# Optimization experiments

Measured on AMD Instinct MI355X. Metric: run time of the kernel, lower is better.

## Reference

```python
import jax, jax.numpy as jnp
import numpy as np

B, M, S = 4, 1024, 1024
D, H, FF = 1024, 16, 4096
NE, P = 128, 1
HD = D // H
EPS = 1e-5


def _layer_norm(x, g, b):
    mu = x.mean(-1, keepdims=True)
    var = ((x - mu) ** 2).mean(-1, keepdims=True)
    return (x - mu) * jax.lax.rsqrt(var + EPS) * g + b


def _mha(q_in, kv_in, in_w, in_b, out_w, out_b):
    # torch nn.MultiheadAttention: packed in_proj_weight [3D, D], y = x @ W.T + b
    wq, wk, wv = in_w[:D], in_w[D:2 * D], in_w[2 * D:]
    bq, bk, bv = in_b[:D], in_b[D:2 * D], in_b[2 * D:]
    q = (q_in @ wq.T + bq).reshape(q_in.shape[0], q_in.shape[1], H, HD)
    k = (kv_in @ wk.T + bk).reshape(kv_in.shape[0], kv_in.shape[1], H, HD)
    v = (kv_in @ wv.T + bv).reshape(kv_in.shape[0], kv_in.shape[1], H, HD)
    scores = jnp.einsum('bqhd,bkhd->bhqk', q, k) / jnp.sqrt(jnp.float32(HD))
    attn = jax.nn.softmax(scores, axis=-1)
    o = jnp.einsum('bhqk,bkhd->bqhd', attn, v).reshape(q_in.shape[0], q_in.shape[1], D)
    return o @ out_w.T + out_b


def _soft_moe(h, phi, exp_w, exp_b):
    # h: [b, m, FF]; phi: [FF, n, p]
    logits = jnp.einsum('bmd,dnp->bmnp', h, phi)
    dispatch = jax.nn.softmax(logits, axis=1)  # over tokens m
    b, m, n, p = logits.shape
    combine = jax.nn.softmax(logits.reshape(b, m, n * p), axis=-1).reshape(b, m, n, p)
    slots = jnp.einsum('bmd,bmnp->bnpd', h, dispatch)  # [b, n, p, FF]
    y = jnp.einsum('bnpd,ndo->bnpo', slots, exp_w) + exp_b[None, :, None, :]  # [b, n, p, D]
    return jnp.einsum('bnpo,bmnp->bmo', y, combine)


def setup_inputs() -> dict:
    key = jax.random.key(0)
    ks = jax.random.split(key, 16)
    sc = 0.02

    def rn(k, shape):
        return jax.random.normal(k, shape, jnp.float32) * sc

    return {
        'tgt': jax.random.normal(ks[0], (B, M, D), jnp.float32),
        'memory': jax.random.normal(ks[1], (B, S, D), jnp.float32),
        'sa_in_w': rn(ks[2], (3 * D, D)), 'sa_in_b': jnp.zeros((3 * D,), jnp.float32),
        'sa_out_w': rn(ks[3], (D, D)), 'sa_out_b': jnp.zeros((D,), jnp.float32),
        'ca_in_w': rn(ks[4], (3 * D, D)), 'ca_in_b': jnp.zeros((3 * D,), jnp.float32),
        'ca_out_w': rn(ks[5], (D, D)), 'ca_out_b': jnp.zeros((D,), jnp.float32),
        'norm1_g': jnp.ones((D,), jnp.float32), 'norm1_b': jnp.zeros((D,), jnp.float32),
        'norm2_g': jnp.ones((D,), jnp.float32), 'norm2_b': jnp.zeros((D,), jnp.float32),
        'norm3_g': jnp.ones((D,), jnp.float32), 'norm3_b': jnp.zeros((D,), jnp.float32),
        'lin_w': rn(ks[6], (FF, D)), 'lin_b': jnp.zeros((FF,), jnp.float32),
        'phi': rn(ks[7], (FF, NE, P)),
        'exp_w': rn(ks[8], (NE, FF, D)), 'exp_b': jnp.zeros((NE, D), jnp.float32),
    }


def reference(tgt, memory, sa_in_w, sa_in_b, sa_out_w, sa_out_b,
              ca_in_w, ca_in_b, ca_out_w, ca_out_b,
              norm1_g, norm1_b, norm2_g, norm2_b, norm3_g, norm3_b,
              lin_w, lin_b, phi, exp_w, exp_b):
    # post-norm (norm_first=False), dropout=0 (eval)
    x = tgt
    x = _layer_norm(x + _mha(x, x, sa_in_w, sa_in_b, sa_out_w, sa_out_b), norm1_g, norm1_b)
    x = _layer_norm(x + _mha(x, memory, ca_in_w, ca_in_b, ca_out_w, ca_out_b), norm2_g, norm2_b)
    h = jax.nn.relu(x @ lin_w.T + lin_b)  # [B, M, FF]
    ff = _soft_moe(h, phi, exp_w, exp_b)  # [B, M, D]
    x = _layer_norm(x + ff, norm3_g, norm3_b)
    return x
```

## Files before the change

### kernel.cpp

```cpp
#include <hip/hip_runtime.h>
#include <cstdint>
#include <cstddef>

typedef unsigned short u16;
typedef unsigned int   u32;
typedef short bf16x8 __attribute__((ext_vector_type(8)));
typedef float f32x4  __attribute__((ext_vector_type(4)));
typedef u16   u16x8  __attribute__((ext_vector_type(8)));
typedef u16   u16x4  __attribute__((ext_vector_type(4)));
typedef u16   u16x2  __attribute__((ext_vector_type(2)));

constexpr int B_  = 4;
constexpr int M_  = 1024;
constexpr int S_  = 1024;
constexpr int D_  = 1024;
constexpr int H_  = 16;
constexpr int FF_ = 4096;
constexpr int NE_ = 128;

__device__ __forceinline__ u16 f2bf(float f) {
    u32 u = __builtin_bit_cast(u32, f);
    u = (u + 0x7fffu + ((u >> 16) & 1u)) >> 16;
    return (u16)u;
}
__device__ __forceinline__ float bf2f(u16 u) {
    u32 x = ((u32)u) << 16;
    return __builtin_bit_cast(float, x);
}
__device__ __forceinline__ void gload_lds16(const u16* g, u16* l) {
    __builtin_amdgcn_global_load_lds(
        (const __attribute__((address_space(1))) u32*)g,
        (__attribute__((address_space(3))) u32*)l, 16, 0, 0);
}

template<int OUT_BF16, int RELU, int HAS_BIAS>
__global__ __launch_bounds__(256) void gemm_bt_mfma(
    const u16* __restrict__ A, const u16* __restrict__ W,
    const float* __restrict__ bias, void* __restrict__ Cout,
    int K, int N, int lda, int ldw,
    size_t sA, size_t sW, size_t sC)
{
    __shared__ u16 As[128 * 32];
    __shared__ u16 Bs[128 * 32];
    const int tid = threadIdx.x;
    const int w = tid >> 6, l = tid & 63;
    const int bm = blockIdx.y * 128, bn = blockIdx.x * 128;
    const u16* Ab = A + (size_t)blockIdx.z * sA;
    const u16* Wb = W + (size_t)blockIdx.z * sW;

    const int wr = w >> 1, wc = w & 1;
    const int sr = l >> 2;
    const int sk = (l & 3) * 8;
    const u16* aG0 = Ab + (size_t)(bm + w * 16 + sr) * lda + sk;
    const u16* aG1 = Ab + (size_t)(bm + (w + 4) * 16 + sr) * lda + sk;
    const u16* bG0 = Wb + (size_t)(bn + w * 16 + sr) * ldw + sk;
    const u16* bG1 = Wb + (size_t)(bn + (w + 4) * 16 + sr) * ldw + sk;
    u16* aL0 = &As[w * 512];
    u16* aL1 = &As[(w + 4) * 512];
    u16* bL0 = &Bs[w * 512];
    u16* bL1 = &Bs[(w + 4) * 512];

    const int fr = l & 15;
    const int fk = (l >> 4) * 8;

    f32x4 acc[4][4];
#pragma unroll
    for (int i = 0; i < 4; ++i)
#pragma unroll
        for (int j = 0; j < 4; ++j)
#pragma unroll
            for (int q = 0; q < 4; ++q) acc[i][j][q] = 0.f;

    for (int k0 = 0; k0 < K; k0 += 32) {
        __syncthreads();
        gload_lds16(aG0, aL0);
        gload_lds16(aG1, aL1);
        gload_lds16(bG0, bL0);
        gload_lds16(bG1, bL1);
        aG0 += 32; aG1 += 32; bG0 += 32; bG1 += 32;
        __syncthreads();
        bf16x8 af[4], bfr[4];
#pragma unroll
        for (int m = 0; m < 4; ++m)
            af[m] = *(const bf16x8*)&As[(wr * 64 + m * 16 + fr) * 32 + fk];
#pragma unroll
        for (int n = 0; n < 4; ++n)
            bfr[n] = *(const bf16x8*)&Bs[(wc * 64 + n * 16 + fr) * 32 + fk];
#pragma unroll
        for (int m = 0; m < 4; ++m)
#pragma unroll
            for (int n = 0; n < 4; ++n)
                acc[m][n] = __builtin_amdgcn_mfma_f32_16x16x32_bf16(
                    af[m], bfr[n], acc[m][n], 0, 0, 0);
    }

    const int row0 = bm + wr * 64 + (l >> 4) * 4;
    const int col0 = bn + wc * 64;
#pragma unroll
    for (int n = 0; n < 4; ++n) {
        const int col = col0 + n * 16 + fr;
        float bv = 0.f;
        if (HAS_BIAS) bv = bias[col];
#pragma unroll
        for (int m = 0; m < 4; ++m) {
            const int row = row0 + m * 16;
#pragma unroll
            for (int j = 0; j < 4; ++j) {
                float v = acc[m][n][j] + bv;
                if (RELU) v = fmaxf(v, 0.f);
                const size_t idx = (size_t)blockIdx.z * sC + (size_t)(row + j) * N + col;
                if (OUT_BF16) ((u16*)Cout)[idx] = f2bf(v);
                else          ((float*)Cout)[idx] = v;
            }
        }
    }
}

__global__ __launch_bounds__(256) void flash_attn_kernel(
    const u16* __restrict__ Q, int qs,
    const u16* __restrict__ K, int ks,
    const u16* __restrict__ V, int vs,
    u16* __restrict__ O, int Slen)
{
    __shared__ u16 Qs[64][72];
    __shared__ u16 Ks[64][72];
    __shared__ u16 Vt[64][72];
    __shared__ u16 Pw[4][16][72];
    const int b = blockIdx.z, hh = blockIdx.y;
    const int m0 = blockIdx.x * 64;
    const int tid = threadIdx.x;
    const int w = tid >> 6, l = tid & 63;
    const int lq = l & 15, g = l >> 4;

    {
        const int row = tid >> 2, cg = (tid & 3) * 16;
        const u16* qp = Q + ((size_t)b * M_ + m0 + row) * qs + hh * 64 + cg;
        u16x8 v0 = *(const u16x8*)qp;
        u16x8 v1 = *(const u16x8*)(qp + 8);
        u16x8 o0, o1;
#pragma unroll
        for (int i = 0; i < 8; ++i) {
            o0[i] = f2bf(bf2f(v0[i]) * 0.125f);
            o1[i] = f2bf(bf2f(v1[i]) * 0.125f);
        }
        *(u16x8*)&Qs[row][cg]     = o0;
        *(u16x8*)&Qs[row][cg + 8] = o1;
    }
    __syncthreads();
    bf16x8 qf[2];
    qf[0] = *(const bf16x8*)&Qs[w * 16 + lq][g * 8];
    qf[1] = *(const bf16x8*)&Qs[w * 16 + lq][32 + g * 8];

    f32x4 acc_o[4];
#pragma unroll
    for (int nb = 0; nb < 4; ++nb)
#pragma unroll
        for (int j = 0; j < 4; ++j) acc_o[nb][j] = 0.f;
    float m_run = -1e30f, l_run = 0.f;

    const int kp = tid & 31, dg = tid >> 5;
    const int krow = tid >> 2, kcg = (tid & 3) * 16;

    for (int s0 = 0; s0 < Slen; s0 += 64) {
        __syncthreads();
        {
            const u16* kpp = K + ((size_t)b * Slen + s0 + krow) * ks + hh * 64 + kcg;
            *(u16x8*)&Ks[krow][kcg]     = *(const u16x8*)kpp;
            *(u16x8*)&Ks[krow][kcg + 8] = *(const u16x8*)(kpp + 8);
        }
        {
            const u16* vp0 = V + ((size_t)b * Slen + s0 + 2 * kp) * vs + hh * 64 + dg * 8;
            const u16* vp1 = vp0 + vs;
            u16x8 a = *(const u16x8*)vp0;
            u16x8 c = *(const u16x8*)vp1;
#pragma unroll
            for (int i = 0; i < 8; ++i) {
                u16x2 pk; pk[0] = a[i]; pk[1] = c[i];
                *(u16x2*)&Vt[dg * 8 + i][2 * kp] = pk;
            }
        }
        __syncthreads();

        f32x4 s4[4];
#pragma unroll
        for (int mb = 0; mb < 4; ++mb) {
            f32x4 z = {0.f, 0.f, 0.f, 0.f};
            bf16x8 a0 = *(const bf16x8*)&Ks[mb * 16 + lq][g * 8];
            bf16x8 a1 = *(const bf16x8*)&Ks[mb * 16 + lq][32 + g * 8];
            z = __builtin_amdgcn_mfma_f32_16x16x32_bf16(a0, qf[0], z, 0, 0, 0);
            z = __builtin_amdgcn_mfma_f32_16x16x32_bf16(a1, qf[1], z, 0, 0, 0);
            s4[mb] = z;
        }

        float pm = -1e30f;
#pragma unroll
        for (int mb = 0; mb < 4; ++mb)
#pragma unroll
            for (int j = 0; j < 4; ++j) pm = fmaxf(pm, s4[mb][j]);
        pm = fmaxf(pm, __shfl_xor(pm, 16));
        pm = fmaxf(pm, __shfl_xor(pm, 32));

        u16 pbf[4][4];
        float ls = 0.f;
        if (__all(pm - m_run <= 8.f)) {
#pragma unroll
            for (int mb = 0; mb < 4; ++mb)
#pragma unroll
                for (int j = 0; j < 4; ++j) {
                    float p = __expf(s4[mb][j] - m_run);
                    ls += p;
                    pbf[mb][j] = f2bf(p);
                }
            ls += __shfl_xor(ls, 16);
            ls += __shfl_xor(ls, 32);
            l_run += ls;
        } else {
            const float m_new = fmaxf(m_run, pm);
            const float alpha = __expf(m_run - m_new);
#pragma unroll
            for (int mb = 0; mb < 4; ++mb)
#pragma unroll
                for (int j = 0; j < 4; ++j) {
                    float p = __expf(s4[mb][j] - m_new);
                    ls += p;
                    pbf[mb][j] = f2bf(p);
                }
            ls += __shfl_xor(ls, 16);
            ls += __shfl_xor(ls, 32);
            l_run = l_run * alpha + ls;
            m_run = m_new;
            float al[4];
#pragma unroll
            for (int j = 0; j < 4; ++j) al[j] = __shfl(alpha, 4 * g + j);
#pragma unroll
            for (int nb = 0; nb < 4; ++nb)
#pragma unroll
                for (int j = 0; j < 4; ++j) acc_o[nb][j] *= al[j];
        }

#pragma unroll
        for (int mb = 0; mb < 4; ++mb) {
            u16x4 pk;
            pk[0] = pbf[mb][0]; pk[1] = pbf[mb][1];
            pk[2] = pbf[mb][2]; pk[3] = pbf[mb][3];
            *(u16x4*)&Pw[w][lq][mb * 16 + g * 4] = pk;
        }

#pragma unroll
        for (int kc = 0; kc < 2; ++kc) {
            bf16x8 pa = *(const bf16x8*)&Pw[w][lq][kc * 32 + g * 8];
#pragma unroll
            for (int nb = 0; nb < 4; ++nb) {
                bf16x8 bv = *(const bf16x8*)&Vt[nb * 16 + lq][kc * 32 + g * 8];
                acc_o[nb] = __builtin_amdgcn_mfma_f32_16x16x32_bf16(pa, bv, acc_o[nb], 0, 0, 0);
            }
        }
    }

    float linv[4];
#pragma unroll
    for (int j = 0; j < 4; ++j) linv[j] = 1.f / __shfl(l_run, 4 * g + j);
#pragma unroll
    for (int nb = 0; nb < 4; ++nb)
#pragma unroll
        for (int j = 0; j < 4; ++j) {
            const size_t row = (size_t)b * M_ + m0 + w * 16 + 4 * g + j;
            O[row * D_ + hh * 64 + nb * 16 + lq] = f2bf(acc_o[nb][j] * linv[j]);
        }
}

__global__ __launch_bounds__(256) void cvt_multi_kernel(
    const float* __restrict__ s0, u16* __restrict__ d0,
    const float* __restrict__ s1, u16* __restrict__ d1,
    const float* __restrict__ s2, u16* __restrict__ d2,
    const float* __restrict__ s3, u16* __restrict__ d3,
    const float* __restrict__ s4, u16* __restrict__ d4,
    const float* __restrict__ s5, u16* __restrict__ d5,
    const float* __restrict__ s6, u16* __restrict__ d6)
{
    int blk = blockIdx.x;
    const float* s; u16* d;
    if      (blk < 2048) { s = s0; d = d0; }
    else if (blk < 4096) { s = s1; d = d1; blk -= 2048; }
    else if (blk < 5632) { s = s2; d = d2; blk -= 4096; }
    else if (blk < 6144) { s = s3; d = d3; blk -= 5632; }
    else if (blk < 7680) { s = s4; d = d4; blk -= 6144; }
    else if (blk < 8192) { s = s5; d = d5; blk -= 7680; }
    else                 { s = s6; d = d6; blk -= 8192; }
    const size_t i = ((size_t)blk * 256 + threadIdx.x) * 8;
    float4 a = *(const float4*)(s + i);
    float4 b = *(const float4*)(s + i + 4);
    u16x8 o;
    o[0] = f2bf(a.x); o[1] = f2bf(a.y); o[2] = f2bf(a.z); o[3] = f2bf(a.w);
    o[4] = f2bf(b.x); o[5] = f2bf(b.y); o[6] = f2bf(b.z); o[7] = f2bf(b.w);
    *(u16x8*)(d + i) = o;
}

__global__ __launch_bounds__(256) void transpose_f32_bf16_kernel(
    const float* __restrict__ src, u16* __restrict__ dst, int R, int C,
    size_t sI, size_t sO)
{
    __shared__ u16 t[32][33];
    src += (size_t)blockIdx.z * sI;
    dst += (size_t)blockIdx.z * sO;
    const int c0 = blockIdx.x * 32, r0 = blockIdx.y * 32;
    const int x = threadIdx.x & 31, y = threadIdx.x >> 5;
    for (int i = y; i < 32; i += 8)
        t[i][x] = f2bf(src[(size_t)(r0 + i) * C + c0 + x]);
    __syncthreads();
    for (int i = y; i < 32; i += 8)
        dst[(size_t)(c0 + i) * R + r0 + x] = t[x][i];
}

__global__ __launch_bounds__(256) void transpose_bf16_kernel(
    const u16* __restrict__ src, u16* __restrict__ dst, int R, int C,
    size_t sI, size_t sO)
{
    __shared__ u16 t[32][33];
    src += (size_t)blockIdx.z * sI;
    dst += (size_t)blockIdx.z * sO;
    const int c0 = blockIdx.x * 32, r0 = blockIdx.y * 32;
    const int x = threadIdx.x & 31, y = threadIdx.x >> 5;
    for (int i = y; i < 32; i += 8)
        t[i][x] = src[(size_t)(r0 + i) * C + c0 + x];
    __syncthreads();
    for (int i = y; i < 32; i += 8)
        dst[(size_t)(c0 + i) * R + r0 + x] = t[x][i];
}

__global__ __launch_bounds__(256) void resid_ln_kernel(
    const float* __restrict__ X, const float* __restrict__ R,
    const float* __restrict__ g, const float* __restrict__ bt,
    float* __restrict__ Y, u16* __restrict__ Ybf)
{
    __shared__ float s1[4], s2[4];
    const size_t row = blockIdx.x;
    const int tid = threadIdx.x;
    const float4 x4 = *(const float4*)(X + row * 1024 + tid * 4);
    const float4 r4 = *(const float4*)(R + row * 1024 + tid * 4);
    float v[4] = {x4.x + r4.x, x4.y + r4.y, x4.z + r4.z, x4.w + r4.w};
    float s = v[0] + v[1] + v[2] + v[3];
    float q = v[0] * v[0] + v[1] * v[1] + v[2] * v[2] + v[3] * v[3];
#pragma unroll
    for (int off = 32; off; off >>= 1) {
        s += __shfl_xor(s, off);
        q += __shfl_xor(q, off);
    }
    if ((tid & 63) == 0) { s1[tid >> 6] = s; s2[tid >> 6] = q; }
    __syncthreads();
    s = s1[0] + s1[1] + s1[2] + s1[3];
    q = s2[0] + s2[1] + s2[2] + s2[3];
    const float mu = s * (1.f / 1024.f);
    const float var = q * (1.f / 1024.f) - mu * mu;
    const float rinv = rsqrtf(var + 1e-5f);
    const float4 g4 = *(const float4*)(g + tid * 4);
    const float4 b4 = *(const float4*)(bt + tid * 4);
    float o[4];
    o[0] = (v[0] - mu) * rinv * g4.x + b4.x;
    o[1] = (v[1] - mu) * rinv * g4.y + b4.y;
    o[2] = (v[2] - mu) * rinv * g4.z + b4.z;
    o[3] = (v[3] - mu) * rinv * g4.w + b4.w;
    *(float4*)(Y + row * 1024 + tid * 4) = *(float4*)o;
    if (Ybf) {
        u16x4 ob;
        ob[0] = f2bf(o[0]); ob[1] = f2bf(o[1]);
        ob[2] = f2bf(o[2]); ob[3] = f2bf(o[3]);
        *(u16x4*)(Ybf + row * 1024 + tid * 4) = ob;
    }
}

__global__ __launch_bounds__(256) void dispatch_softmax_T_kernel(
    const float* __restrict__ logitsP, u16* __restrict__ dispT)
{
    __shared__ float red[4];
    constexpr size_t CH = (size_t)B_ * M_ * NE_;
    const int n = blockIdx.x, b = blockIdx.y;
    u16* O = dispT + ((size_t)b * NE_ + n) * M_;
    const int tid = threadIdx.x;
    float v[4];
#pragma unroll
    for (int i = 0; i < 4; ++i) {
        const size_t idx = (size_t)(b * M_ + tid + 256 * i) * NE_ + n;
        v[i] = logitsP[idx] + logitsP[CH + idx] + logitsP[2 * CH + idx] + logitsP[3 * CH + idx];
    }
    float mx = fmaxf(fmaxf(v[0], v[1]), fmaxf(v[2], v[3]));
#pragma unroll
    for (int off = 32; off; off >>= 1) mx = fmaxf(mx, __shfl_xor(mx, off));
    if ((tid & 63) == 0) red[tid >> 6] = mx;
    __syncthreads();
    mx = fmaxf(fmaxf(red[0], red[1]), fmaxf(red[2], red[3]));
    __syncthreads();
    float e[4], s = 0.f;
#pragma unroll
    for (int i = 0; i < 4; ++i) { e[i] = __expf(v[i] - mx); s += e[i]; }
#pragma unroll
    for (int off = 32; off; off >>= 1) s += __shfl_xor(s, off);
    if ((tid & 63) == 0) red[tid >> 6] = s;
    __syncthreads();
    s = red[0] + red[1] + red[2] + red[3];
    const float inv = 1.f / s;
#pragma unroll
    for (int i = 0; i < 4; ++i) O[tid + 256 * i] = f2bf(e[i] * inv);
}

__global__ __launch_bounds__(64) void combine_softmax_kernel(
    const float* __restrict__ logitsP, u16* __restrict__ comb)
{
    constexpr size_t CH = (size_t)B_ * M_ * NE_;
    const size_t row = blockIdx.x;
    const int lane = threadIdx.x;
    const size_t i0 = row * NE_ + lane;
    const size_t i1 = i0 + 64;
    float a = logitsP[i0] + logitsP[CH + i0] + logitsP[2 * CH + i0] + logitsP[3 * CH + i0];
    float c = logitsP[i1] + logitsP[CH + i1] + logitsP[2 * CH + i1] + logitsP[3 * CH + i1];
    float mx = fmaxf(a, c);
#pragma unroll
    for (int off = 32; off; off >>= 1) mx = fmaxf(mx, __shfl_xor(mx, off));
    float e0 = __expf(a - mx), e1 = __expf(c - mx);
    float s = e0 + e1;
#pragma unroll
    for (int off = 32; off; off >>= 1) s += __shfl_xor(s, off);
    const float inv = 1.f / s;
    comb[row * NE_ + lane]      = f2bf(e0 * inv);
    comb[row * NE_ + lane + 64] = f2bf(e1 * inv);
}

__global__ __launch_bounds__(256) void expert_partial_kernel(
    const float* __restrict__ slots, const float* __restrict__ exp_w,
    float* __restrict__ part)
{
    __shared__ float sl[4][512];
    const int n = blockIdx.x;
    const int c = blockIdx.y;
    const int f0 = c * 512;
    const int t = threadIdx.x;
    for (int i = t; i < 2048; i += 256) {
        const int b = i >> 9, f = i & 511;
        sl[b][f] = slots[((size_t)b * NE_ + n) * FF_ + f0 + f];
    }
    __syncthreads();
    const int d4 = t * 4;
    const float* wp = exp_w + ((size_t)n * FF_ + f0) * D_ + d4;
    f32x4 acc[4];
#pragma unroll
    for (int b = 0; b < 4; ++b)
#pragma unroll
        for (int j = 0; j < 4; ++j) acc[b][j] = 0.f;
#pragma unroll 4
    for (int f = 0; f < 512; ++f) {
        const float4 w4 = *(const float4*)wp;
        wp += D_;
#pragma unroll
        for (int b = 0; b < 4; ++b) {
            const float s = sl[b][f];
            acc[b][0] = fmaf(s, w4.x, acc[b][0]);
            acc[b][1] = fmaf(s, w4.y, acc[b][1]);
            acc[b][2] = fmaf(s, w4.z, acc[b][2]);
            acc[b][3] = fmaf(s, w4.w, acc[b][3]);
        }
    }
#pragma unroll
    for (int b = 0; b < 4; ++b)
        *(f32x4*)&part[(((size_t)c * 4 + b) * NE_ + n) * D_ + d4] = acc[b];
}

__global__ __launch_bounds__(256) void reduce_yT_kernel(
    const float* __restrict__ part, const float* __restrict__ exp_b,
    u16* __restrict__ yT)
{
    __shared__ float tile[32][33];
    const int d0 = blockIdx.x * 32, n0 = blockIdx.y * 32, b = blockIdx.z;
    const int x = threadIdx.x & 31, y = threadIdx.x >> 5;
    for (int i = y; i < 32; i += 8) {
        const int n = n0 + i;
        float s = exp_b[(size_t)n * D_ + d0 + x];
#pragma unroll
        for (int c = 0; c < 8; ++c)
            s += part[(((size_t)c * 4 + b) * NE_ + n) * D_ + d0 + x];
        tile[i][x] = s;
    }
    __syncthreads();
    for (int i = y; i < 32; i += 8)
        yT[((size_t)b * D_ + d0 + i) * NE_ + n0 + x] = f2bf(tile[x][i]);
}

extern "C" void kernel_launch(void* const* d_in, const int* in_sizes, int n_in,
                              void* d_out, int out_size, void* d_ws, size_t ws_size,
                              hipStream_t stream)
{
    const float* tgt      = (const float*)d_in[0];
    const float* memry    = (const float*)d_in[1];
    const float* sa_in_w  = (const float*)d_in[2];
    const float* sa_in_b  = (const float*)d_in[3];
    const float* sa_out_w = (const float*)d_in[4];
    const float* sa_out_b = (const float*)d_in[5];
    const float* ca_in_w  = (const float*)d_in[6];
    const float* ca_in_b  = (const float*)d_in[7];
    const float* ca_out_w = (const float*)d_in[8];
    const float* ca_out_b = (const float*)d_in[9];
    const float* norm1_g  = (const float*)d_in[10];
    const float* norm1_b  = (const float*)d_in[11];
    const float* norm2_g  = (const float*)d_in[12];
    const float* norm2_b  = (const float*)d_in[13];
    const float* norm3_g  = (const float*)d_in[14];
    const float* norm3_b  = (const float*)d_in[15];
    const float* lin_w    = (const float*)d_in[16];
    const float* lin_b    = (const float*)d_in[17];
    const float* phi      = (const float*)d_in[18];
    const float* exp_w    = (const float*)d_in[19];
    const float* exp_b    = (const float*)d_in[20];

    float* ws = (float*)d_ws;
    u16*   qkv_bf  = (u16*)(ws);
    float* proj    = ws + 6291456;
    float* x1      = ws + 10485760;
    float* x2      = ws + 14680064;
    float* logitsP = ws + 18874368;
    float* part    = ws + 20971520;
    u16*   h_bf    = (u16*)(ws + 25165824);
    u16*   hT_bf   = (u16*)(ws + 33554432);
    u16*   obuf_bf = (u16*)(ws + 41943040);
    u16*   x1_bf   = (u16*)(ws + 44040192);
    u16*   x2_bf   = (u16*)(ws + 46137344);
    u16*   tgt_bf  = (u16*)(ws + 48234496);
    u16*   mem_bf  = (u16*)(ws + 50331648);
    u16*   dispT   = (u16*)(ws + 52428800);
    u16*   comb_bf = (u16*)(ws + 52690944);
    u16*   yT_bf   = (u16*)(ws + 52953088);
    u16*   slots_n = 0; float* slots = ws + 53215232;
    (void)slots_n;
    u16*   w_sa_in = (u16*)(ws + 55312384);
    u16*   w_sa_out= (u16*)(ws + 56885248);
    u16*   w_ca_in = (u16*)(ws + 57409536);
    u16*   w_ca_out= (u16*)(ws + 58982400);
    u16*   w_lin   = (u16*)(ws + 59506688);
    u16*   phiT    = (u16*)(ws + 61603840);

    cvt_multi_kernel<<<10240, 256, 0, stream>>>(
        tgt, tgt_bf, memry, mem_bf, sa_in_w, w_sa_in, sa_out_w, w_sa_out,
        ca_in_w, w_ca_in, ca_out_w, w_ca_out, lin_w, w_lin);
    transpose_f32_bf16_kernel<<<dim3(4, 128, 1), 256, 0, stream>>>(phi, phiT, 4096, 128, 0, 0);

    gemm_bt_mfma<1, 0, 1><<<dim3(24, 32, 1), 256, 0, stream>>>(
        tgt_bf, w_sa_in, sa_in_b, qkv_bf, 1024, 3072, 1024, 1024, 0, 0, 0);
    flash_attn_kernel<<<dim3(16, 16, 4), 256, 0, stream>>>(
        qkv_bf, 3072, qkv_bf + 1024, 3072, qkv_bf + 2048, 3072, obuf_bf, S_);
    gemm_bt_mfma<0, 0, 1><<<dim3(8, 32, 1), 256, 0, stream>>>(
        obuf_bf, w_sa_out, sa_out_b, proj, 1024, 1024, 1024, 1024, 0, 0, 0);
    resid_ln_kernel<<<4096, 256, 0, stream>>>(tgt, proj, norm1_g, norm1_b, x1, x1_bf);

    u16* qca_bf = qkv_bf;
    u16* kvca_bf = qkv_bf + (size_t)4096 * 1024;
    gemm_bt_mfma<1, 0, 1><<<dim3(8, 32, 1), 256, 0, stream>>>(
        x1_bf, w_ca_in, ca_in_b, qca_bf, 1024, 1024, 1024, 1024, 0, 0, 0);
    gemm_bt_mfma<1, 0, 1><<<dim3(16, 32, 1), 256, 0, stream>>>(
        mem_bf, w_ca_in + (size_t)1024 * 1024, ca_in_b + 1024,
        kvca_bf, 1024, 2048, 1024, 1024, 0, 0, 0);
    flash_attn_kernel<<<dim3(16, 16, 4), 256, 0, stream>>>(
        qca_bf, 1024, kvca_bf, 2048, kvca_bf + 1024, 2048, obuf_bf, S_);
    gemm_bt_mfma<0, 0, 1><<<dim3(8, 32, 1), 256, 0, stream>>>(
        obuf_bf, w_ca_out, ca_out_b, proj, 1024, 1024, 1024, 1024, 0, 0, 0);
    resid_ln_kernel<<<4096, 256, 0, stream>>>(x1, proj, norm2_g, norm2_b, x2, x2_bf);

    gemm_bt_mfma<1, 1, 1><<<dim3(32, 32, 1), 256, 0, stream>>>(
        x2_bf, w_lin, lin_b, h_bf, 1024, 4096, 1024, 1024, 0, 0, 0);
    gemm_bt_mfma<0, 0, 0><<<dim3(1, 32, 4), 256, 0, stream>>>(
        h_bf, phiT, nullptr, logitsP, 1024, 128, 4096, 4096,
        1024, 1024, (size_t)B_ * M_ * NE_);
    dispatch_softmax_T_kernel<<<dim3(NE_, B_), 256, 0, stream>>>(logitsP, dispT);
    combine_softmax_kernel<<<dim3(B_ * M_), 64, 0, stream>>>(logitsP, comb_bf);
    transpose_bf16_kernel<<<dim3(128, 32, 4), 256, 0, stream>>>(
        h_bf, hT_bf, 1024, 4096, (size_t)M_ * FF_, (size_t)M_ * FF_);
    gemm_bt_mfma<0, 0, 0><<<dim3(32, 1, 4), 256, 0, stream>>>(
        dispT, hT_bf, nullptr, slots, 1024, 4096, 1024, 1024,
        (size_t)NE_ * M_, (size_t)FF_ * M_, (size_t)NE_ * FF_);
    expert_partial_kernel<<<dim3(NE_, 8), 256, 0, stream>>>(slots, exp_w, part);
    reduce_yT_kernel<<<dim3(32, 4, 4), 256, 0, stream>>>(part, exp_b, yT_bf);
    gemm_bt_mfma<0, 0, 0><<<dim3(8, 8, 4), 256, 0, stream>>>(
        comb_bf, yT_bf, nullptr, proj, 128, 1024, 128, 128,
        (size_t)M_ * NE_, (size_t)D_ * NE_, (size_t)M_ * D_);
    resid_ln_kernel<<<4096, 256, 0, stream>>>(x2, proj, norm3_g, norm3_b,
                                              (float*)d_out, nullptr);
}
```

Baseline: 839.0 us.

## Use 64x128 GEMM tiles with swizzled LDS, fuse h transpose, double-buffer attention

The GEMM kernel now uses 64-row by 128-column tiles with an XOR-swizzled LDS layout to reduce bank conflicts, and the grids are doubled to give more blocks per launch. The linear+ReLU GEMM also writes a transposed bf16 copy of h directly, which removes the separate transpose kernel and its extra pass over memory. Flash attention keeps Q in registers instead of staging it through LDS and double-buffers the K/V tiles, prefetching the next tile into registers while the current one is computed. In exchange, the smaller tiles lower per-block data reuse, and the transposed store in the GEMM epilogue is strided.

```diff
diff --git a/kernel.cpp b/kernel.cpp
--- a/kernel.cpp
+++ b/kernel.cpp
@@ -33,84 +33,86 @@
         (__attribute__((address_space(3))) u32*)l, 16, 0, 0);
 }
 
-template<int OUT_BF16, int RELU, int HAS_BIAS>
-__global__ __launch_bounds__(256) void gemm_bt_mfma(
+template<int OUT_BF16, int RELU, int HAS_BIAS, int WRITE_HT>
+__global__ __launch_bounds__(256) void gemm64_mfma(
     const u16* __restrict__ A, const u16* __restrict__ W,
     const float* __restrict__ bias, void* __restrict__ Cout,
+    u16* __restrict__ HT,
     int K, int N, int lda, int ldw,
     size_t sA, size_t sW, size_t sC)
 {
-    __shared__ u16 As[128 * 32];
+    __shared__ u16 As[64 * 32];
     __shared__ u16 Bs[128 * 32];
     const int tid = threadIdx.x;
     const int w = tid >> 6, l = tid & 63;
-    const int bm = blockIdx.y * 128, bn = blockIdx.x * 128;
+    const int fr = l & 15, g = l >> 4;
+    const int bm = blockIdx.y * 64, bn = blockIdx.x * 128;
     const u16* Ab = A + (size_t)blockIdx.z * sA;
     const u16* Wb = W + (size_t)blockIdx.z * sW;
 
-    const int wr = w >> 1, wc = w & 1;
-    const int sr = l >> 2;
-    const int sk = (l & 3) * 8;
-    const u16* aG0 = Ab + (size_t)(bm + w * 16 + sr) * lda + sk;
-    const u16* aG1 = Ab + (size_t)(bm + (w + 4) * 16 + sr) * lda + sk;
-    const u16* bG0 = Wb + (size_t)(bn + w * 16 + sr) * ldw + sk;
-    const u16* bG1 = Wb + (size_t)(bn + (w + 4) * 16 + sr) * ldw + sk;
-    u16* aL0 = &As[w * 512];
-    u16* aL1 = &As[(w + 4) * 512];
+    const int qcol = ((l & 3) ^ ((l >> 3) & 3)) * 8;
+    const int srow = w * 16 + (l >> 2);
+    const u16* aG  = Ab + (size_t)(bm + srow) * lda + qcol;
+    const u16* bG0 = Wb + (size_t)(bn + srow) * ldw + qcol;
+    const u16* bG1 = bG0 + (size_t)64 * ldw;
+    u16* aL  = &As[w * 512];
     u16* bL0 = &Bs[w * 512];
-    u16* bL1 = &Bs[(w + 4) * 512];
-
-    const int fr = l & 15;
-    const int fk = (l >> 4) * 8;
-
-    f32x4 acc[4][4];
-#pragma unroll
-    for (int i = 0; i < 4; ++i)
-#pragma unroll
-        for (int j = 0; j < 4; ++j)
-#pragma unroll
-            for (int q = 0; q < 4; ++q) acc[i][j][q] = 0.f;
+    u16* bL1 = &Bs[2048 + w * 512];
+
+    const int qsw = (g ^ ((fr >> 1) & 3)) * 8;
+
+    f32x4 acc[4][2];
+#pragma unroll
+    for (int m = 0; m < 4; ++m)
+#pragma unroll
+        for (int n = 0; n < 2; ++n)
+#pragma unroll
+            for (int q = 0; q < 4; ++q) acc[m][n][q] = 0.f;
 
     for (int k0 = 0; k0 < K; k0 += 32) {
         __syncthreads();
-        gload_lds16(aG0, aL0);
-        gload_lds16(aG1, aL1);
+        gload_lds16(aG,  aL);
         gload_lds16(bG0, bL0);
         gload_lds16(bG1, bL1);
-        aG0 += 32; aG1 += 32; bG0 += 32; bG1 += 32;
+        aG += 32; bG0 += 32; bG1 += 32;
         __syncthreads();
-        bf16x8 af[4], bfr[4];
+        bf16x8 af[4], bf[2];
 #pragma unroll
         for (int m = 0; m < 4; ++m)
-            af[m] = *(const bf16x8*)&As[(wr * 64 + m * 16 + fr) * 32 + fk];
-#pragma unroll
-        for (int n = 0; n < 4; ++n)
-            bfr[n] = *(const bf16x8*)&Bs[(wc * 64 + n * 16 + fr) * 32 + fk];
+            af[m] = *(const bf16x8*)&As[(m * 16 + fr) * 32 + qsw];
+#pragma unroll
+        for (int n = 0; n < 2; ++n)
+            bf[n] = *(const bf16x8*)&Bs[(w * 32 + n * 16 + fr) * 32 + qsw];
 #pragma unroll
         for (int m = 0; m < 4; ++m)
 #pragma unroll
-            for (int n = 0; n < 4; ++n)
+            for (int n = 0; n < 2; ++n)
                 acc[m][n] = __builtin_amdgcn_mfma_f32_16x16x32_bf16(
-                    af[m], bfr[n], acc[m][n], 0, 0, 0);
-    }
-
-    const int row0 = bm + wr * 64 + (l >> 4) * 4;
-    const int col0 = bn + wc * 64;
-#pragma unroll
-    for (int n = 0; n < 4; ++n) {
-        const int col = col0 + n * 16 + fr;
+                    af[m], bf[n], acc[m][n], 0, 0, 0);
+    }
+
+    const int row0 = bm + g * 4;
+#pragma unroll
+    for (int n = 0; n < 2; ++n) {
+        const int col = bn + w * 32 + n * 16 + fr;
         float bv = 0.f;
         if (HAS_BIAS) bv = bias[col];
 #pragma unroll
         for (int m = 0; m < 4; ++m) {
-            const int row = row0 + m * 16;
+            const int rowm = row0 + m * 16;
+            u16 o[4];
 #pragma unroll
             for (int j = 0; j < 4; ++j) {
                 float v = acc[m][n][j] + bv;
                 if (RELU) v = fmaxf(v, 0.f);
-                const size_t idx = (size_t)blockIdx.z * sC + (size_t)(row + j) * N + col;
-                if (OUT_BF16) ((u16*)Cout)[idx] = f2bf(v);
-                else          ((float*)Cout)[idx] = v;
+                const size_t idx = (size_t)blockIdx.z * sC +
+                                   (size_t)(rowm + j) * N + col;
+                if (OUT_BF16) { o[j] = f2bf(v); ((u16*)Cout)[idx] = o[j]; }
+                else          { ((float*)Cout)[idx] = v; }
+            }
+            if (WRITE_HT) {
+                u16x4 pk; pk[0] = o[0]; pk[1] = o[1]; pk[2] = o[2]; pk[3] = o[3];
+                *(u16x4*)&HT[(((size_t)(rowm >> 10)) * N + col) * 1024 + (rowm & 1023)] = pk;
             }
         }
     }
@@ -122,9 +124,8 @@
     const u16* __restrict__ V, int vs,
     u16* __restrict__ O, int Slen)
 {
-    __shared__ u16 Qs[64][72];
-    __shared__ u16 Ks[64][72];
-    __shared__ u16 Vt[64][72];
+    __shared__ u16 Ks[2][64][72];
+    __shared__ u16 Vt[2][64][72];
     __shared__ u16 Pw[4][16][72];
     const int b = blockIdx.z, hh = blockIdx.y;
     const int m0 = blockIdx.x * 64;
@@ -132,24 +133,20 @@
     const int w = tid >> 6, l = tid & 63;
     const int lq = l & 15, g = l >> 4;
 
+    bf16x8 qf[2];
     {
-        const int row = tid >> 2, cg = (tid & 3) * 16;
-        const u16* qp = Q + ((size_t)b * M_ + m0 + row) * qs + hh * 64 + cg;
-        u16x8 v0 = *(const u16x8*)qp;
-        u16x8 v1 = *(const u16x8*)(qp + 8);
+        const u16* qp = Q + ((size_t)b * M_ + m0 + w * 16 + lq) * qs + hh * 64;
+        u16x8 v0 = *(const u16x8*)(qp + g * 8);
+        u16x8 v1 = *(const u16x8*)(qp + 32 + g * 8);
         u16x8 o0, o1;
 #pragma unroll
         for (int i = 0; i < 8; ++i) {
             o0[i] = f2bf(bf2f(v0[i]) * 0.125f);
             o1[i] = f2bf(bf2f(v1[i]) * 0.125f);
         }
-        *(u16x8*)&Qs[row][cg]     = o0;
-        *(u16x8*)&Qs[row][cg + 8] = o1;
-    }
-    __syncthreads();
-    bf16x8 qf[2];
-    qf[0] = *(const bf16x8*)&Qs[w * 16 + lq][g * 8];
-    qf[1] = *(const bf16x8*)&Qs[w * 16 + lq][32 + g * 8];
+        qf[0] = __builtin_bit_cast(bf16x8, o0);
+        qf[1] = __builtin_bit_cast(bf16x8, o1);
+    }
 
     f32x4 acc_o[4];
 #pragma unroll
@@ -161,32 +158,42 @@
     const int kp = tid & 31, dg = tid >> 5;
     const int krow = tid >> 2, kcg = (tid & 3) * 16;
 
-    for (int s0 = 0; s0 < Slen; s0 += 64) {
-        __syncthreads();
-        {
-            const u16* kpp = K + ((size_t)b * Slen + s0 + krow) * ks + hh * 64 + kcg;
-            *(u16x8*)&Ks[krow][kcg]     = *(const u16x8*)kpp;
-            *(u16x8*)&Ks[krow][kcg + 8] = *(const u16x8*)(kpp + 8);
-        }
-        {
-            const u16* vp0 = V + ((size_t)b * Slen + s0 + 2 * kp) * vs + hh * 64 + dg * 8;
-            const u16* vp1 = vp0 + vs;
-            u16x8 a = *(const u16x8*)vp0;
-            u16x8 c = *(const u16x8*)vp1;
-#pragma unroll
-            for (int i = 0; i < 8; ++i) {
-                u16x2 pk; pk[0] = a[i]; pk[1] = c[i];
-                *(u16x2*)&Vt[dg * 8 + i][2 * kp] = pk;
-            }
-        }
-        __syncthreads();
+    const int nt = Slen >> 6;
+    u16x8 kv0, kv1, va, vb;
+
+#define ATT_LOAD(T_)                                                          \
+    {                                                                         \
+        const u16* kpp = K + ((size_t)b * Slen + (T_) * 64 + krow) * ks + hh * 64 + kcg; \
+        kv0 = *(const u16x8*)kpp;                                             \
+        kv1 = *(const u16x8*)(kpp + 8);                                       \
+        const u16* vp0 = V + ((size_t)b * Slen + (T_) * 64 + 2 * kp) * vs + hh * 64 + dg * 8; \
+        va = *(const u16x8*)vp0;                                              \
+        vb = *(const u16x8*)(vp0 + vs);                                       \
+    }
+#define ATT_WRITE(BUF_)                                                       \
+    {                                                                         \
+        *(u16x8*)&Ks[BUF_][krow][kcg]     = kv0;                              \
+        *(u16x8*)&Ks[BUF_][krow][kcg + 8] = kv1;                              \
+        _Pragma("unroll") for (int i = 0; i < 8; ++i) {                       \
+            u16x2 pk; pk[0] = va[i]; pk[1] = vb[i];                           \
+            *(u16x2*)&Vt[BUF_][dg * 8 + i][2 * kp] = pk;                      \
+        }                                                                     \
+    }
+
+    ATT_LOAD(0)
+    ATT_WRITE(0)
+    __syncthreads();
+
+    for (int t = 0; t < nt; ++t) {
+        if (t + 1 < nt) ATT_LOAD(t + 1)
+        const int cb = t & 1;
 
         f32x4 s4[4];
 #pragma unroll
         for (int mb = 0; mb < 4; ++mb) {
             f32x4 z = {0.f, 0.f, 0.f, 0.f};
-            bf16x8 a0 = *(const bf16x8*)&Ks[mb * 16 + lq][g * 8];
-            bf16x8 a1 = *(const bf16x8*)&Ks[mb * 16 + lq][32 + g * 8];
+            bf16x8 a0 = *(const bf16x8*)&Ks[cb][mb * 16 + lq][g * 8];
+            bf16x8 a1 = *(const bf16x8*)&Ks[cb][mb * 16 + lq][32 + g * 8];
             z = __builtin_amdgcn_mfma_f32_16x16x32_bf16(a0, qf[0], z, 0, 0, 0);
             z = __builtin_amdgcn_mfma_f32_16x16x32_bf16(a1, qf[1], z, 0, 0, 0);
             s4[mb] = z;
@@ -251,11 +258,16 @@
             bf16x8 pa = *(const bf16x8*)&Pw[w][lq][kc * 32 + g * 8];
 #pragma unroll
             for (int nb = 0; nb < 4; ++nb) {
-                bf16x8 bv = *(const bf16x8*)&Vt[nb * 16 + lq][kc * 32 + g * 8];
+                bf16x8 bv = *(const bf16x8*)&Vt[cb][nb * 16 + lq][kc * 32 + g * 8];
                 acc_o[nb] = __builtin_amdgcn_mfma_f32_16x16x32_bf16(pa, bv, acc_o[nb], 0, 0, 0);
             }
         }
-    }
+
+        if (t + 1 < nt) ATT_WRITE((t + 1) & 1)
+        __syncthreads();
+    }
+#undef ATT_LOAD
+#undef ATT_WRITE
 
     float linv[4];
 #pragma unroll
@@ -307,22 +319,6 @@
     const int x = threadIdx.x & 31, y = threadIdx.x >> 5;
     for (int i = y; i < 32; i += 8)
         t[i][x] = f2bf(src[(size_t)(r0 + i) * C + c0 + x]);
-    __syncthreads();
-    for (int i = y; i < 32; i += 8)
-        dst[(size_t)(c0 + i) * R + r0 + x] = t[x][i];
-}
-
-__global__ __launch_bounds__(256) void transpose_bf16_kernel(
-    const u16* __restrict__ src, u16* __restrict__ dst, int R, int C,
-    size_t sI, size_t sO)
-{
-    __shared__ u16 t[32][33];
-    src += (size_t)blockIdx.z * sI;
-    dst += (size_t)blockIdx.z * sO;
-    const int c0 = blockIdx.x * 32, r0 = blockIdx.y * 32;
-    const int x = threadIdx.x & 31, y = threadIdx.x >> 5;
-    for (int i = y; i < 32; i += 8)
-        t[i][x] = src[(size_t)(r0 + i) * C + c0 + x];
     __syncthreads();
     for (int i = y; i < 32; i += 8)
         dst[(size_t)(c0 + i) * R + r0 + x] = t[x][i];
@@ -527,8 +523,7 @@
     u16*   dispT   = (u16*)(ws + 52428800);
     u16*   comb_bf = (u16*)(ws + 52690944);
     u16*   yT_bf   = (u16*)(ws + 52953088);
-    u16*   slots_n = 0; float* slots = ws + 53215232;
-    (void)slots_n;
+    float* slots   = ws + 53215232;
     u16*   w_sa_in = (u16*)(ws + 55312384);
     u16*   w_sa_out= (u16*)(ws + 56885248);
     u16*   w_ca_in = (u16*)(ws + 57409536);
@@ -536,48 +531,48 @@
     u16*   w_lin   = (u16*)(ws + 59506688);
     u16*   phiT    = (u16*)(ws + 61603840);
 
+    constexpr size_t CH = (size_t)B_ * M_ * NE_;
+
     cvt_multi_kernel<<<10240, 256, 0, stream>>>(
         tgt, tgt_bf, memry, mem_bf, sa_in_w, w_sa_in, sa_out_w, w_sa_out,
         ca_in_w, w_ca_in, ca_out_w, w_ca_out, lin_w, w_lin);
     transpose_f32_bf16_kernel<<<dim3(4, 128, 1), 256, 0, stream>>>(phi, phiT, 4096, 128, 0, 0);
 
-    gemm_bt_mfma<1, 0, 1><<<dim3(24, 32, 1), 256, 0, stream>>>(
-        tgt_bf, w_sa_in, sa_in_b, qkv_bf, 1024, 3072, 1024, 1024, 0, 0, 0);
+    gemm64_mfma<1, 0, 1, 0><<<dim3(24, 64, 1), 256, 0, stream>>>(
+        tgt_bf, w_sa_in, sa_in_b, qkv_bf, nullptr, 1024, 3072, 1024, 1024, 0, 0, 0);
     flash_attn_kernel<<<dim3(16, 16, 4), 256, 0, stream>>>(
         qkv_bf, 3072, qkv_bf + 1024, 3072, qkv_bf + 2048, 3072, obuf_bf, S_);
-    gemm_bt_mfma<0, 0, 1><<<dim3(8, 32, 1), 256, 0, stream>>>(
-        obuf_bf, w_sa_out, sa_out_b, proj, 1024, 1024, 1024, 1024, 0, 0, 0);
+    gemm64_mfma<0, 0, 1, 0><<<dim3(8, 64, 1), 256, 0, stream>>>(
+        obuf_bf, w_sa_out, sa_out_b, proj, nullptr, 1024, 1024, 1024, 1024, 0, 0, 0);
     resid_ln_kernel<<<4096, 256, 0, stream>>>(tgt, proj, norm1_g, norm1_b, x1, x1_bf);
 
     u16* qca_bf = qkv_bf;
     u16* kvca_bf = qkv_bf + (size_t)4096 * 1024;
-    gemm_bt_mfma<1, 0, 1><<<dim3(8, 32, 1), 256, 0, stream>>>(
-        x1_bf, w_ca_in, ca_in_b, qca_bf, 1024, 1024, 1024, 1024, 0, 0, 0);
-    gemm_bt_mfma<1, 0, 1><<<dim3(16, 32, 1), 256, 0, stream>>>(
+    gemm64_mfma<1, 0, 1, 0><<<dim3(8, 64, 1), 256, 0, stream>>>(
+        x1_bf, w_ca_in, ca_in_b, qca_bf, nullptr, 1024, 1024, 1024, 1024, 0, 0, 0);
+    gemm64_mfma<1, 0, 1, 0><<<dim3(16, 64, 1), 256, 0, stream>>>(
         mem_bf, w_ca_in + (size_t)1024 * 1024, ca_in_b + 1024,
-        kvca_bf, 1024, 2048, 1024, 1024, 0, 0, 0);
+        kvca_bf, nullptr, 1024, 2048, 1024, 1024, 0, 0, 0);
     flash_attn_kernel<<<dim3(16, 16, 4), 256, 0, stream>>>(
         qca_bf, 1024, kvca_bf, 2048, kvca_bf + 1024, 2048, obuf_bf, S_);
-    gemm_bt_mfma<0, 0, 1><<<dim3(8, 32, 1), 256, 0, stream>>>(
-        obuf_bf, w_ca_out, ca_out_b, proj, 1024, 1024, 1024, 1024, 0, 0, 0);
+    gemm64_mfma<0, 0, 1, 0><<<dim3(8, 64, 1), 256, 0, stream>>>(
+        obuf_bf, w_ca_out, ca_out_b, proj, nullptr, 1024, 1024, 1024, 1024, 0, 0, 0);
     resid_ln_kernel<<<4096, 256, 0, stream>>>(x1, proj, norm2_g, norm2_b, x2, x2_bf);
 
-    gemm_bt_mfma<1, 1, 1><<<dim3(32, 32, 1), 256, 0, stream>>>(
-        x2_bf, w_lin, lin_b, h_bf, 1024, 4096, 1024, 1024, 0, 0, 0);
-    gemm_bt_mfma<0, 0, 0><<<dim3(1, 32, 4), 256, 0, stream>>>(
-        h_bf, phiT, nullptr, logitsP, 1024, 128, 4096, 4096,
-        1024, 1024, (size_t)B_ * M_ * NE_);
+    gemm64_mfma<1, 1, 1, 1><<<dim3(32, 64, 1), 256, 0, stream>>>(
+        x2_bf, w_lin, lin_b, h_bf, hT_bf, 1024, 4096, 1024, 1024, 0, 0, 0);
+    gemm64_mfma<0, 0, 0, 0><<<dim3(1, 64, 4), 256, 0, stream>>>(
+        h_bf, phiT, nullptr, logitsP, nullptr, 1024, 128, 4096, 4096,
+        1024, 1024, CH);
     dispatch_softmax_T_kernel<<<dim3(NE_, B_), 256, 0, stream>>>(logitsP, dispT);
     combine_softmax_kernel<<<dim3(B_ * M_), 64, 0, stream>>>(logitsP, comb_bf);
-    transpose_bf16_kernel<<<dim3(128, 32, 4), 256, 0, stream>>>(
-        h_bf, hT_bf, 1024, 4096, (size_t)M_ * FF_, (size_t)M_ * FF_);
-    gemm_bt_mfma<0, 0, 0><<<dim3(32, 1, 4), 256, 0, stream>>>(
-        dispT, hT_bf, nullptr, slots, 1024, 4096, 1024, 1024,
+    gemm64_mfma<0, 0, 0, 0><<<dim3(32, 2, 4), 256, 0, stream>>>(
+        dispT, hT_bf, nullptr, slots, nullptr, 1024, 4096, 1024, 1024,
         (size_t)NE_ * M_, (size_t)FF_ * M_, (size_t)NE_ * FF_);
     expert_partial_kernel<<<dim3(NE_, 8), 256, 0, stream>>>(slots, exp_w, part);
     reduce_yT_kernel<<<dim3(32, 4, 4), 256, 0, stream>>>(part, exp_b, yT_bf);
-    gemm_bt_mfma<0, 0, 0><<<dim3(8, 8, 4), 256, 0, stream>>>(
-        comb_bf, yT_bf, nullptr, proj, 128, 1024, 128, 128,
+    gemm64_mfma<0, 0, 0, 0><<<dim3(8, 16, 4), 256, 0, stream>>>(
+        comb_bf, yT_bf, nullptr, proj, nullptr, 128, 1024, 128, 128,
         (size_t)M_ * NE_, (size_t)D_ * NE_, (size_t)M_ * D_);
     resid_ln_kernel<<<4096, 256, 0, stream>>>(x2, proj, norm3_g, norm3_b,
                                               (float*)d_out, nullptr);
```

Measured after the change: 821.4 us. 2.1% less time.
